# Kernel optimization log

Hardware: AMD Instinct MI355X
Metric: run time of the kernel (lower is better)

## Reference

```python
import jax, jax.numpy as jnp
import numpy as np

NUM_HEADS = 32
NUM_KV_HEADS = 8
HEAD_DIM = 128
HIDDEN = 4096
ROPE_THETA = 10000.0
SLIDING_WINDOW = 1024
NEG_INF = -1e9


def _make_sliding_window_mask(q_len, kv_len, window):
    # additive mask: 0 where attendable (causal AND within window), -inf otherwise
    i = jnp.arange(q_len)[:, None]
    j = jnp.arange(kv_len)[None, :]
    allowed = (j <= i) & (j > i - window)
    return jnp.where(allowed, 0.0, NEG_INF).astype(jnp.float32)[None, None]  # [1,1,q,kv]


def _rope_tables(seq_len, head_dim, theta):
    inv_freq = 1.0 / (theta ** (jnp.arange(0, head_dim, 2, dtype=jnp.float32) / head_dim))
    t = jnp.arange(seq_len, dtype=jnp.float32)
    freqs = jnp.einsum('i,j->ij', t, inv_freq)        # [S, D/2]
    emb = jnp.concatenate([freqs, freqs], axis=-1)     # [S, D]
    return jnp.cos(emb), jnp.sin(emb)


def _rotate_half(x):
    d = x.shape[-1] // 2
    return jnp.concatenate([-x[..., d:], x[..., :d]], axis=-1)


def setup_inputs() -> dict:
    key = jax.random.key(0)
    ks = jax.random.split(key, 5)
    B, S = 1, 2048
    sc = 0.02
    hidden_states = jax.random.normal(ks[0], (B, S, HIDDEN), dtype=jnp.float32)
    Wq = jax.random.normal(ks[1], (HIDDEN, NUM_HEADS * HEAD_DIM), dtype=jnp.float32) * sc
    Wk = jax.random.normal(ks[2], (HIDDEN, NUM_KV_HEADS * HEAD_DIM), dtype=jnp.float32) * sc
    Wv = jax.random.normal(ks[3], (HIDDEN, NUM_KV_HEADS * HEAD_DIM), dtype=jnp.float32) * sc
    Wo = jax.random.normal(ks[4], (NUM_HEADS * HEAD_DIM, HIDDEN), dtype=jnp.float32) * sc
    attention_mask = _make_sliding_window_mask(S, S, SLIDING_WINDOW)
    position_ids = jnp.arange(S, dtype=jnp.int64)[None, :]
    return {"hidden_states": hidden_states, "attention_mask": attention_mask,
            "position_ids": position_ids, "Wq": Wq, "Wk": Wk, "Wv": Wv, "Wo": Wo}


def reference(hidden_states, attention_mask, position_ids, Wq, Wk, Wv, Wo):
    B, S, _ = hidden_states.shape
    # projections
    q = (hidden_states @ Wq).reshape(B, S, NUM_HEADS, HEAD_DIM).transpose(0, 2, 1, 3)      # [B,H,S,D]
    k = (hidden_states @ Wk).reshape(B, S, NUM_KV_HEADS, HEAD_DIM).transpose(0, 2, 1, 3)   # [B,Hk,S,D]
    v = (hidden_states @ Wv).reshape(B, S, NUM_KV_HEADS, HEAD_DIM).transpose(0, 2, 1, 3)
    # RoPE
    cos_t, sin_t = _rope_tables(S, HEAD_DIM, ROPE_THETA)
    cos = cos_t[position_ids][:, None]  # [B,1,S,D]
    sin = sin_t[position_ids][:, None]
    q = q * cos + _rotate_half(q) * sin
    k = k * cos + _rotate_half(k) * sin
    # repeat_kv (GQA): [B,Hk,S,D] -> [B,H,S,D]
    n_rep = NUM_HEADS // NUM_KV_HEADS
    k = jnp.repeat(k, n_rep, axis=1)
    v = jnp.repeat(v, n_rep, axis=1)
    # attention
    scores = jnp.einsum('bhqd,bhkd->bhqk', q, k) / np.sqrt(HEAD_DIM)
    scores = scores + attention_mask
    probs = jax.nn.softmax(scores, axis=-1)
    out = jnp.einsum('bhqk,bhkd->bhqd', probs, v)
    out = out.transpose(0, 2, 1, 3).reshape(B, S, HIDDEN)
    return out @ Wo
```

## Files before the change

### kernel.cpp

```cpp
#include <hip/hip_runtime.h>

typedef __attribute__((ext_vector_type(8))) short short8;
typedef __attribute__((ext_vector_type(4))) short s16x4;
typedef __attribute__((ext_vector_type(4))) float f32x4;
typedef unsigned short u16;
typedef unsigned int u32;

__device__ __forceinline__ u16 f2bf(float f) {
  union { float f; unsigned int u; } v; v.f = f;
  unsigned int r = (v.u + 0x7FFFu + ((v.u >> 16) & 1u)) >> 16;
  return (u16)r;
}
__device__ __forceinline__ float bf2f(u16 b) {
  union { unsigned int u; float f; } v; v.u = ((unsigned int)b) << 16;
  return v.f;
}
__device__ __forceinline__ void load_lds16(const void* g, void* l) {
  __builtin_amdgcn_global_load_lds((const __attribute__((address_space(1))) void*)g,
                                   (__attribute__((address_space(3))) void*)l, 16, 0, 0);
}

__global__ void cvt_f32_bf16_kernel(const float* __restrict__ in, u16* __restrict__ out, int n4) {
  int i = blockIdx.x * blockDim.x + threadIdx.x;
  if (i >= n4) return;
  float4 v = ((const float4*)in)[i];
  ushort4 o;
  o.x = f2bf(v.x); o.y = f2bf(v.y); o.z = f2bf(v.z); o.w = f2bf(v.w);
  ((ushort4*)out)[i] = o;
}

__global__ void combine2_f32_kernel(float* __restrict__ out, const u16* __restrict__ p0,
                                    const u16* __restrict__ p1, int n8) {
  int i = blockIdx.x * blockDim.x + threadIdx.x;
  if (i >= n8) return;
  short8 a = ((const short8*)p0)[i];
  short8 b = ((const short8*)p1)[i];
  float4 o0, o1;
  o0.x = bf2f((u16)a[0]) + bf2f((u16)b[0]);
  o0.y = bf2f((u16)a[1]) + bf2f((u16)b[1]);
  o0.z = bf2f((u16)a[2]) + bf2f((u16)b[2]);
  o0.w = bf2f((u16)a[3]) + bf2f((u16)b[3]);
  o1.x = bf2f((u16)a[4]) + bf2f((u16)b[4]);
  o1.y = bf2f((u16)a[5]) + bf2f((u16)b[5]);
  o1.z = bf2f((u16)a[6]) + bf2f((u16)b[6]);
  o1.w = bf2f((u16)a[7]) + bf2f((u16)b[7]);
  ((float4*)out)[i * 2]     = o0;
  ((float4*)out)[i * 2 + 1] = o1;
}

__global__ void combine_kv_rope_kernel(const u16* __restrict__ PKV, u16* __restrict__ Kb,
                                       u16* __restrict__ Vt) {
  int i = blockIdx.x * blockDim.x + threadIdx.x;
  if (i < 131072) {
    int s = i >> 6, r = i & 63, hh = r >> 3, c = r & 7;
    size_t lo8 = (size_t)s * 128 + hh * 16 + c;
    size_t hi8 = lo8 + 8;
    float lo[8] = {0,0,0,0,0,0,0,0}, hi[8] = {0,0,0,0,0,0,0,0};
#pragma unroll
    for (int z = 0; z < 4; ++z) {
      short8 a = *(const short8*)(PKV + (size_t)z * 4194304 + lo8 * 8);
      short8 b = *(const short8*)(PKV + (size_t)z * 4194304 + hi8 * 8);
#pragma unroll
      for (int j = 0; j < 8; ++j) { lo[j] += bf2f((u16)a[j]); hi[j] += bf2f((u16)b[j]); }
    }
    short8 olo, ohi;
#pragma unroll
    for (int ii = 0; ii < 8; ++ii) {
      int j = c * 8 + ii;
      float invf = exp2f(-(float)j * (13.287712379549449f / 64.0f));
      float sn, cs;
      sincosf((float)s * invf, &sn, &cs);
      olo[ii] = (short)f2bf(lo[ii] * cs - hi[ii] * sn);
      ohi[ii] = (short)f2bf(hi[ii] * cs + lo[ii] * sn);
    }
    *(short8*)(Kb + lo8 * 8) = olo;
    *(short8*)(Kb + hi8 * 8) = ohi;
  } else {
    int v = i - 131072;
    const u16* src = PKV + 2097152;
    float sm[8] = {0,0,0,0,0,0,0,0};
#pragma unroll
    for (int z = 0; z < 4; ++z) {
      short8 a = *(const short8*)(src + (size_t)z * 4194304 + (size_t)v * 8);
#pragma unroll
      for (int j = 0; j < 8; ++j) sm[j] += bf2f((u16)a[j]);
    }
    short8 o;
#pragma unroll
    for (int j = 0; j < 8; ++j) o[j] = (short)f2bf(sm[j]);
    ((short8*)Vt)[v] = o;
  }
}

__device__ __forceinline__ void tconv64_tile(const float* __restrict__ W, u16* __restrict__ Wt,
                                             int K, int N, int nb, int kb, int tid) {
  __shared__ float tile[64][65];
  int tx = tid & 15, ty = tid >> 4;
  const float* src = W + (size_t)(kb + ty) * N + nb + tx * 4;
#pragma unroll
  for (int i = 0; i < 4; ++i) {
    float4 v = *(const float4*)(src + (size_t)i * 16 * N);
    tile[ty + i * 16][tx * 4 + 0] = v.x;
    tile[ty + i * 16][tx * 4 + 1] = v.y;
    tile[ty + i * 16][tx * 4 + 2] = v.z;
    tile[ty + i * 16][tx * 4 + 3] = v.w;
  }
  __syncthreads();
  u16* dst = Wt + (size_t)(nb + ty) * K + kb + tx * 4;
#pragma unroll
  for (int i = 0; i < 4; ++i) {
    s16x4 o;
#pragma unroll
    for (int j = 0; j < 4; ++j) o[j] = (short)f2bf(tile[tx * 4 + j][ty + i * 16]);
    *(s16x4*)(dst + (size_t)i * 16 * K) = o;
  }
}

__global__ void tconv3_kernel(const float* __restrict__ Wq, const float* __restrict__ Wk,
                              const float* __restrict__ Wv, u16* __restrict__ WqT,
                              u16* __restrict__ WkvT) {
  int id = blockIdx.x;
  if (id < 4096)      tconv64_tile(Wq, WqT, 4096, 4096, (id & 63) * 64, (id >> 6) * 64, threadIdx.x);
  else if (id < 5120) { int t = id - 4096; tconv64_tile(Wk, WkvT, 4096, 1024, (t & 15) * 64, (t >> 4) * 64, threadIdx.x); }
  else                { int t = id - 5120; tconv64_tile(Wv, WkvT + (size_t)1024 * 4096, 4096, 1024, (t & 15) * 64, (t >> 4) * 64, threadIdx.x); }
}

__global__ void tconv1_kernel(const float* __restrict__ W, u16* __restrict__ Wt) {
  int id = blockIdx.x;
  tconv64_tile(W, Wt, 4096, 4096, (id & 63) * 64, (id >> 6) * 64, threadIdx.x);
}

__global__ __launch_bounds__(512, 1) void gemm256_kernel(
    const u16* __restrict__ A, const u16* __restrict__ B,
    u16* __restrict__ C0, u16* __restrict__ C1, int N, int K, int KH) {
  __shared__ u16 As[2][256 * 64];
  __shared__ u16 Bs[2][256 * 64];
  int tid = threadIdx.x, lane = tid & 63, wid = tid >> 6;
  int wr = wid >> 2, wc = wid & 3;
  int g = lane >> 4, q = lane & 15;
  int id = blockIdx.z * gridDim.x * gridDim.y + blockIdx.y * gridDim.x + blockIdx.x;
  int tot = gridDim.x * gridDim.y * gridDim.z;
  int swz = (id & 7) * (tot >> 3) + (id >> 3);
  int perh = gridDim.x * gridDim.y;
  int z = swz / perh, rem = swz % perh;
  int m0 = (rem / gridDim.x) * 256, n0 = (rem % gridDim.x) * 256;
  int k0 = z * KH;
  f32x4 acc[8][4];
#pragma unroll
  for (int i = 0; i < 8; ++i)
#pragma unroll
    for (int j = 0; j < 4; ++j) acc[i][j] = (f32x4){0.f, 0.f, 0.f, 0.f};
  int srow = tid >> 3;
  int scol = ((tid & 7) ^ (srow & 7)) << 3;
  const u16* ga = A + (size_t)(m0 + srow) * K + k0 + scol;
  const u16* gb = B + (size_t)(n0 + srow) * K + k0 + scol;
  int xorm = (q & 7) << 3;
  int arow = wr * 128 + q;
  int brow = wc * 64 + q;
  int nt = KH >> 6;

  auto stage = [&](int buf, int t) {
    const u16* pa = ga + t * 64;
    const u16* pb = gb + t * 64;
#pragma unroll
    for (int it = 0; it < 4; ++it) {
      load_lds16(pa + (size_t)it * 64 * K, (char*)(&As[buf][0]) + it * 8192 + tid * 16);
      load_lds16(pb + (size_t)it * 64 * K, (char*)(&Bs[buf][0]) + it * 8192 + tid * 16);
    }
  };

  stage(0, 0);
  stage(1, 1);
  asm volatile("s_waitcnt vmcnt(8)" ::: "memory");
  __builtin_amdgcn_s_barrier();
  for (int t = 0; t < nt; ++t) {
    int cur = t & 1;
    int col0 = (g * 8) ^ xorm;
    short8 a0[8], b0[4];
#pragma unroll
    for (int m = 0; m < 8; ++m) a0[m] = *(const short8*)&As[cur][(arow + m * 16) * 64 + col0];
#pragma unroll
    for (int n = 0; n < 4; ++n) b0[n] = *(const short8*)&Bs[cur][(brow + n * 16) * 64 + col0];
    __builtin_amdgcn_s_setprio(1);
#pragma unroll
    for (int m = 0; m < 8; ++m)
#pragma unroll
      for (int n = 0; n < 4; ++n)
        acc[m][n] = __builtin_amdgcn_mfma_f32_16x16x32_bf16(a0[m], b0[n], acc[m][n], 0, 0, 0);
    __builtin_amdgcn_s_setprio(0);
    int col1 = (32 + g * 8) ^ xorm;
    short8 a1[8], b1[4];
#pragma unroll
    for (int m = 0; m < 8; ++m) a1[m] = *(const short8*)&As[cur][(arow + m * 16) * 64 + col1];
#pragma unroll
    for (int n = 0; n < 4; ++n) b1[n] = *(const short8*)&Bs[cur][(brow + n * 16) * 64 + col1];
    asm volatile("s_waitcnt lgkmcnt(0)" ::: "memory");
    __builtin_amdgcn_s_barrier();
    if (t + 2 < nt) stage(cur, t + 2);
    __builtin_amdgcn_sched_barrier(0);
    __builtin_amdgcn_s_setprio(1);
#pragma unroll
    for (int m = 0; m < 8; ++m)
#pragma unroll
      for (int n = 0; n < 4; ++n)
        acc[m][n] = __builtin_amdgcn_mfma_f32_16x16x32_bf16(a1[m], b1[n], acc[m][n], 0, 0, 0);
    __builtin_amdgcn_s_setprio(0);
    if (t + 2 < nt)      { asm volatile("s_waitcnt vmcnt(8)" ::: "memory"); }
    else if (t + 1 < nt) { asm volatile("s_waitcnt vmcnt(0)" ::: "memory"); }
    __builtin_amdgcn_s_barrier();
  }
  int crow = m0 + wr * 128 + g * 4;
  int ccol = n0 + wc * 64 + q;
  u16* dst = z ? C1 : C0;
#pragma unroll
  for (int fm = 0; fm < 8; ++fm)
#pragma unroll
    for (int fn = 0; fn < 4; ++fn)
#pragma unroll
      for (int r = 0; r < 4; ++r)
        dst[(size_t)(crow + fm * 16 + r) * N + ccol + fn * 16] = f2bf(acc[fm][fn][r]);
}

__global__ __launch_bounds__(512, 1) void gemm_kv256_kernel(
    const u16* __restrict__ A, const u16* __restrict__ B,
    u16* __restrict__ PKV, int K, int KH) {
  __shared__ u16 As[2][256 * 64];
  __shared__ u16 Bs[2][256 * 64];
  int tid = threadIdx.x, lane = tid & 63, wid = tid >> 6;
  int wr = wid >> 2, wc = wid & 3;
  int g = lane >> 4, q = lane & 15;
  int id = blockIdx.z * 64 + blockIdx.y * 8 + blockIdx.x;
  int swz = (id & 7) * 32 + (id >> 3);
  int z = swz >> 6, rem = swz & 63;
  int m0 = (rem >> 3) * 256, n0 = (rem & 7) * 256;
  int k0 = z * KH;
  f32x4 acc[8][4];
#pragma unroll
  for (int i = 0; i < 8; ++i)
#pragma unroll
    for (int j = 0; j < 4; ++j) acc[i][j] = (f32x4){0.f, 0.f, 0.f, 0.f};
  int srow = tid >> 3;
  int scol = ((tid & 7) ^ (srow & 7)) << 3;
  const u16* ga = A + (size_t)(m0 + srow) * K + k0 + scol;
  const u16* gb = B + (size_t)(n0 + srow) * K + k0 + scol;
  int xorm = (q & 7) << 3;
  int arow = wr * 128 + q;
  int brow = wc * 64 + q;
  int nt = KH >> 6;

  auto stage = [&](int buf, int t) {
    const u16* pa = ga + t * 64;
    const u16* pb = gb + t * 64;
#pragma unroll
    for (int it = 0; it < 4; ++it) {
      load_lds16(pa + (size_t)it * 64 * K, (char*)(&As[buf][0]) + it * 8192 + tid * 16);
      load_lds16(pb + (size_t)it * 64 * K, (char*)(&Bs[buf][0]) + it * 8192 + tid * 16);
    }
  };

  stage(0, 0);
  stage(1, 1);
  asm volatile("s_waitcnt vmcnt(8)" ::: "memory");
  __builtin_amdgcn_s_barrier();
  for (int t = 0; t < nt; ++t) {
    int cur = t & 1;
    int col0 = (g * 8) ^ xorm;
    short8 a0[8], b0[4];
#pragma unroll
    for (int m = 0; m < 8; ++m) a0[m] = *(const short8*)&As[cur][(arow + m * 16) * 64 + col0];
#pragma unroll
    for (int n = 0; n < 4; ++n) b0[n] = *(const short8*)&Bs[cur][(brow + n * 16) * 64 + col0];
    __builtin_amdgcn_s_setprio(1);
#pragma unroll
    for (int m = 0; m < 8; ++m)
#pragma unroll
      for (int n = 0; n < 4; ++n)
        acc[m][n] = __builtin_amdgcn_mfma_f32_16x16x32_bf16(a0[m], b0[n], acc[m][n], 0, 0, 0);
    __builtin_amdgcn_s_setprio(0);
    int col1 = (32 + g * 8) ^ xorm;
    short8 a1[8], b1[4];
#pragma unroll
    for (int m = 0; m < 8; ++m) a1[m] = *(const short8*)&As[cur][(arow + m * 16) * 64 + col1];
#pragma unroll
    for (int n = 0; n < 4; ++n) b1[n] = *(const short8*)&Bs[cur][(brow + n * 16) * 64 + col1];
    asm volatile("s_waitcnt lgkmcnt(0)" ::: "memory");
    __builtin_amdgcn_s_barrier();
    if (t + 2 < nt) stage(cur, t + 2);
    __builtin_amdgcn_sched_barrier(0);
    __builtin_amdgcn_s_setprio(1);
#pragma unroll
    for (int m = 0; m < 8; ++m)
#pragma unroll
      for (int n = 0; n < 4; ++n)
        acc[m][n] = __builtin_amdgcn_mfma_f32_16x16x32_bf16(a1[m], b1[n], acc[m][n], 0, 0, 0);
    __builtin_amdgcn_s_setprio(0);
    if (t + 2 < nt)      { asm volatile("s_waitcnt vmcnt(8)" ::: "memory"); }
    else if (t + 1 < nt) { asm volatile("s_waitcnt vmcnt(0)" ::: "memory"); }
    __builtin_amdgcn_s_barrier();
  }
  int crow = m0 + wr * 128 + g * 4;
  int ccol = n0 + wc * 64 + q;
  u16* Kpart = PKV + (size_t)z * 4194304;
  u16* Vpart = Kpart + 2097152;
  if (n0 < 1024) {
#pragma unroll
    for (int fm = 0; fm < 8; ++fm)
#pragma unroll
      for (int fn = 0; fn < 4; ++fn)
#pragma unroll
        for (int r = 0; r < 4; ++r)
          Kpart[(size_t)(crow + fm * 16 + r) * 1024 + ccol + fn * 16] = f2bf(acc[fm][fn][r]);
  } else {
#pragma unroll
    for (int fn = 0; fn < 4; ++fn) {
      int vcol = ccol + fn * 16 - 1024;
#pragma unroll
      for (int fm = 0; fm < 8; ++fm) {
        s16x4 o;
#pragma unroll
        for (int r = 0; r < 4; ++r) o[r] = (short)f2bf(acc[fm][fn][r]);
        *(s16x4*)(Vpart + (size_t)vcol * 2048 + crow + fm * 16) = o;
      }
    }
  }
}

__global__ __launch_bounds__(512, 4) void attn_kernel(
    const u16* __restrict__ Q0, const u16* __restrict__ Q1,
    const u16* __restrict__ Kg, const u16* __restrict__ Vt, u16* __restrict__ O) {
  __shared__ u16 Ks[2][64 * 128];
  __shared__ u16 Vs[2][128 * 64];
  int tid = threadIdx.x, lane = tid & 63, w = tid >> 6;
  int wg = w >> 2;
  int g = lane >> 4, q = lane & 15;
  int q0 = blockIdx.x * 128;
  int h = blockIdx.y, hk = h >> 2;
  int qbase = q0 + wg * 64;
  int qrow = qbase + (w & 3) * 16;
  int xorm = (lane & 7) << 3;
  short8 qf[4];
  {
    size_t qoff = (size_t)(qrow + q) * 4096 + h * 128 + g * 8;
    float sum[4][8];
#pragma unroll
    for (int kk = 0; kk < 4; ++kk) {
      short8 a = *(const short8*)(Q0 + qoff + kk * 32);
      short8 b = *(const short8*)(Q1 + qoff + kk * 32);
#pragma unroll
      for (int i = 0; i < 8; ++i) sum[kk][i] = bf2f((u16)a[i]) + bf2f((u16)b[i]);
    }
    const float scale = 0.12751781828987514f;
    float srow = (float)(qrow + q);
#pragma unroll
    for (int kk = 0; kk < 2; ++kk)
#pragma unroll
      for (int i = 0; i < 8; ++i) {
        int j = kk * 32 + g * 8 + i;
        float invf = exp2f(-(float)j * (13.287712379549449f / 64.0f));
        float sn, cs;
        sincosf(srow * invf, &sn, &cs);
        float lo = sum[kk][i], hi = sum[kk + 2][i];
        qf[kk][i]     = (short)f2bf((lo * cs - hi * sn) * scale);
        qf[kk + 2][i] = (short)f2bf((hi * cs + lo * sn) * scale);
      }
  }
  float mrow = -1e30f, lsum = 0.f;
  f32x4 of[8];
#pragma unroll
  for (int d = 0; d < 8; ++d) of[d] = (f32x4){0.f, 0.f, 0.f, 0.f};
  int bjt_lo = (q0 >= 1024) ? ((q0 - 1023) >> 6) : 0;
  int bjt_hi = (q0 + 64) >> 6;
  int wjt_lo = (qbase >= 1024) ? ((qbase - 1023) >> 6) : 0;
  int wjt_hi = qbase >> 6;
  int krow = tid >> 4;
  int kchunk = (tid & 15) ^ (krow & 7);
  const u16* kbase = Kg + (size_t)krow * 1024 + hk * 128 + (kchunk << 3);
  int vrow = tid >> 3;
  int vchunk = (tid & 7) ^ (vrow & 7);
  const u16* vbase = Vt + (size_t)(hk * 128 + vrow) * 2048 + (vchunk << 3);

  auto stageK = [&](int buf, int j0) {
    const u16* gp = kbase + (size_t)j0 * 1024;
#pragma unroll
    for (int it = 0; it < 2; ++it)
      load_lds16(gp + (size_t)it * 32 * 1024, (char*)(&Ks[buf][0]) + it * 8192 + tid * 16);
  };
  auto stageV = [&](int buf, int j0) {
    const u16* gp = vbase + j0;
#pragma unroll
    for (int it = 0; it < 2; ++it)
      load_lds16(gp + (size_t)it * 64 * 2048, (char*)(&Vs[buf][0]) + it * 8192 + tid * 16);
  };

  int cur = 0;
  stageK(0, bjt_lo << 6);
  stageV(0, bjt_lo << 6);
  asm volatile("s_waitcnt vmcnt(0)" ::: "memory");
  __syncthreads();
  for (int jt = bjt_lo; jt <= bjt_hi; ++jt) {
    int j0 = jt << 6;
    if (jt < bjt_hi) { stageK(cur ^ 1, j0 + 64); stageV(cur ^ 1, j0 + 64); }
    if (jt >= wjt_lo && jt <= wjt_hi) {
      f32x4 sf[4];
#pragma unroll
      for (int nt = 0; nt < 4; ++nt) sf[nt] = (f32x4){0.f, 0.f, 0.f, 0.f};
      const u16* ks = &Ks[cur][0];
      __builtin_amdgcn_s_setprio(1);
#pragma unroll
      for (int kk = 0; kk < 4; ++kk) {
        short8 qv = qf[kk];
        int col = (kk * 32 + g * 8) ^ xorm;
#pragma unroll
        for (int nt = 0; nt < 4; ++nt) {
          short8 kf = *(const short8*)&ks[(nt * 16 + q) * 128 + col];
          sf[nt] = __builtin_amdgcn_mfma_f32_16x16x32_bf16(kf, qv, sf[nt], 0, 0, 0);
        }
      }
      __builtin_amdgcn_s_setprio(0);
      float p[4][4];
#pragma unroll
      for (int nt = 0; nt < 4; ++nt)
#pragma unroll
        for (int r = 0; r < 4; ++r) p[nt][r] = sf[nt][r];
      if (j0 + 63 > qrow || j0 + 1009 <= qrow) {
        int qq = qrow + q;
        int kb = j0 + g * 4;
#pragma unroll
        for (int nt = 0; nt < 4; ++nt)
#pragma unroll
          for (int r = 0; r < 4; ++r) {
            int key = kb + nt * 16 + r;
            if (key > qq || key + 1024 <= qq) p[nt][r] = -1e9f;
          }
      }
      float tm = p[0][0];
#pragma unroll
      for (int nt = 0; nt < 4; ++nt)
#pragma unroll
        for (int r = 0; r < 4; ++r) tm = fmaxf(tm, p[nt][r]);
      tm = fmaxf(tm, __shfl_xor(tm, 16));
      tm = fmaxf(tm, __shfl_xor(tm, 32));
      if (__any(tm > mrow + 8.f)) {
        float nm = fmaxf(mrow, tm);
        float sc = __builtin_amdgcn_exp2f(mrow - nm);
        mrow = nm;
        lsum *= sc;
#pragma unroll
        for (int d = 0; d < 8; ++d) of[d] *= sc;
      }
      float ps = 0.f;
#pragma unroll
      for (int nt = 0; nt < 4; ++nt)
#pragma unroll
        for (int r = 0; r < 4; ++r) {
          float e = __builtin_amdgcn_exp2f(p[nt][r] - mrow);
          p[nt][r] = e;
          ps += e;
        }
      ps += __shfl_xor(ps, 16);
      ps += __shfl_xor(ps, 32);
      lsum += ps;
      u32 pk[4][2];
#pragma unroll
      for (int nt = 0; nt < 4; ++nt) {
        pk[nt][0] = __builtin_amdgcn_perm(__float_as_uint(p[nt][1]), __float_as_uint(p[nt][0]), 0x07060302u);
        pk[nt][1] = __builtin_amdgcn_perm(__float_as_uint(p[nt][3]), __float_as_uint(p[nt][2]), 0x07060302u);
      }
      int s0 = q + ((g & 1) ? 32 : 0);
      int s1 = s0 + 16;
      bool hi_sel = g >= 2;
      const u16* vs = &Vs[cur][0];
      __builtin_amdgcn_s_setprio(1);
#pragma unroll
      for (int kh = 0; kh < 2; ++kh) {
        int lo = kh * 2, hi = lo + 1;
        u32 a0 = (u32)__shfl((int)pk[lo][0], s0);
        u32 a1 = (u32)__shfl((int)pk[lo][1], s0);
        u32 b0 = (u32)__shfl((int)pk[hi][0], s0);
        u32 b1 = (u32)__shfl((int)pk[hi][1], s0);
        u32 a2 = (u32)__shfl((int)pk[lo][0], s1);
        u32 a3 = (u32)__shfl((int)pk[lo][1], s1);
        u32 b2 = (u32)__shfl((int)pk[hi][0], s1);
        u32 b3 = (u32)__shfl((int)pk[hi][1], s1);
        union { u32 u[4]; short8 s; } pb;
        pb.u[0] = hi_sel ? b0 : a0;
        pb.u[1] = hi_sel ? b1 : a1;
        pb.u[2] = hi_sel ? b2 : a2;
        pb.u[3] = hi_sel ? b3 : a3;
        int col = (kh * 32 + g * 8) ^ xorm;
#pragma unroll
        for (int dt = 0; dt < 8; ++dt) {
          short8 vv = *(const short8*)&vs[(dt * 16 + q) * 64 + col];
          of[dt] = __builtin_amdgcn_mfma_f32_16x16x32_bf16(vv, pb.s, of[dt], 0, 0, 0);
        }
      }
      __builtin_amdgcn_s_setprio(0);
    }
    asm volatile("s_waitcnt vmcnt(0)" ::: "memory");
    __builtin_amdgcn_s_barrier();
    cur ^= 1;
  }
  float inv = 1.f / lsum;
  u16* op = O + (size_t)(qrow + q) * 4096 + h * 128 + g * 4;
#pragma unroll
  for (int dt = 0; dt < 8; ++dt) {
    s16x4 o4;
#pragma unroll
    for (int r = 0; r < 4; ++r) o4[r] = (short)f2bf(of[dt][r] * inv);
    *(s16x4*)(op + dt * 16) = o4;
  }
}

extern "C" void kernel_launch(void* const* d_in, const int* in_sizes, int n_in,
                              void* d_out, int out_size, void* d_ws, size_t ws_size,
                              hipStream_t stream) {
  (void)in_sizes; (void)n_in; (void)out_size;
  const float* hs = (const float*)d_in[0];
  const float* Wq = (const float*)d_in[3];
  const float* Wk = (const float*)d_in[4];
  const float* Wv = (const float*)d_in[5];
  const float* Wo = (const float*)d_in[6];
  float* out = (float*)d_out;
  char* ws = (char*)d_ws;

  u16* Xb   = (u16*)(ws + 0);
  u16* Wt   = (u16*)(ws + 16777216);
  u16* WkvT = (u16*)(ws + 50331648);
  u16* Qb   = (u16*)(ws + 67108864);
  u16* Kb   = (u16*)(ws + 83886080);
  u16* Vtb  = (u16*)(ws + 88080384);
  u16* P1q  = (u16*)(ws + 96468992);
  u16* PKV  = Wt;
  u16* P0o  = WkvT;
  u16* P1o  = Qb;
  u16* Ao   = Xb;
  if (ws_size < 113246208u) return;

  cvt_f32_bf16_kernel<<<dim3(2097152 / 256), 256, 0, stream>>>(hs, Xb, 2097152);

  tconv3_kernel<<<dim3(6144), 256, 0, stream>>>(Wq, Wk, Wv, Wt, WkvT);

  gemm256_kernel<<<dim3(16, 8, 2), 512, 0, stream>>>(Xb, Wt, Qb, P1q, 4096, 4096, 2048);

  gemm_kv256_kernel<<<dim3(8, 8, 4), 512, 0, stream>>>(Xb, WkvT, PKV, 4096, 1024);
  combine_kv_rope_kernel<<<dim3(1536), 256, 0, stream>>>(PKV, Kb, Vtb);

  attn_kernel<<<dim3(16, 32), 512, 0, stream>>>(Qb, P1q, Kb, Vtb, Ao);

  tconv1_kernel<<<dim3(4096), 256, 0, stream>>>(Wo, Wt);
  gemm256_kernel<<<dim3(16, 8, 2), 512, 0, stream>>>(Ao, Wt, P0o, P1o, 4096, 4096, 2048);
  combine2_f32_kernel<<<dim3(4096), 256, 0, stream>>>(out, P0o, P1o, 1048576);
}
```

Before: 303.8 us.

## Precompute RoPE cos/sin table, merge prep kernels, hoist K/V staging before Q setup

Result: no change. 299.8 us (-1.3%).

```diff
diff --git a/kernel.cpp b/kernel.cpp
--- a/kernel.cpp
+++ b/kernel.cpp
@@ -20,13 +20,61 @@
                                    (__attribute__((address_space(3))) void*)l, 16, 0, 0);
 }
 
-__global__ void cvt_f32_bf16_kernel(const float* __restrict__ in, u16* __restrict__ out, int n4) {
-  int i = blockIdx.x * blockDim.x + threadIdx.x;
-  if (i >= n4) return;
-  float4 v = ((const float4*)in)[i];
-  ushort4 o;
-  o.x = f2bf(v.x); o.y = f2bf(v.y); o.z = f2bf(v.z); o.w = f2bf(v.w);
-  ((ushort4*)out)[i] = o;
+__device__ __forceinline__ void tconv64_tile(const float* __restrict__ W, u16* __restrict__ Wt,
+                                             int K, int N, int nb, int kb, int tid) {
+  __shared__ float tile[64][65];
+  int tx = tid & 15, ty = tid >> 4;
+  const float* src = W + (size_t)(kb + ty) * N + nb + tx * 4;
+#pragma unroll
+  for (int i = 0; i < 4; ++i) {
+    float4 v = *(const float4*)(src + (size_t)i * 16 * N);
+    tile[ty + i * 16][tx * 4 + 0] = v.x;
+    tile[ty + i * 16][tx * 4 + 1] = v.y;
+    tile[ty + i * 16][tx * 4 + 2] = v.z;
+    tile[ty + i * 16][tx * 4 + 3] = v.w;
+  }
+  __syncthreads();
+  u16* dst = Wt + (size_t)(nb + ty) * K + kb + tx * 4;
+#pragma unroll
+  for (int i = 0; i < 4; ++i) {
+    s16x4 o;
+#pragma unroll
+    for (int j = 0; j < 4; ++j) o[j] = (short)f2bf(tile[tx * 4 + j][ty + i * 16]);
+    *(s16x4*)(dst + (size_t)i * 16 * K) = o;
+  }
+}
+
+__global__ void prep_kernel(const float* __restrict__ Wq, const float* __restrict__ Wk,
+                            const float* __restrict__ Wv, u16* __restrict__ WqT,
+                            u16* __restrict__ WkvT, const float* __restrict__ X,
+                            u16* __restrict__ Xb, float* __restrict__ Tab) {
+  int id = blockIdx.x;
+  int tid = threadIdx.x;
+  if (id < 4096) { tconv64_tile(Wq, WqT, 4096, 4096, (id & 63) * 64, (id >> 6) * 64, tid); return; }
+  if (id < 5120) { int t = id - 4096; tconv64_tile(Wk, WkvT, 4096, 1024, (t & 15) * 64, (t >> 4) * 64, tid); return; }
+  if (id < 6144) { int t = id - 5120; tconv64_tile(Wv, WkvT + (size_t)1024 * 4096, 4096, 1024, (t & 15) * 64, (t >> 4) * 64, tid); return; }
+  if (id < 14336) {
+    int i = (id - 6144) * 256 + tid;
+    float4 v = ((const float4*)X)[i];
+    ushort4 o;
+    o.x = f2bf(v.x); o.y = f2bf(v.y); o.z = f2bf(v.z); o.w = f2bf(v.w);
+    ((ushort4*)Xb)[i] = o;
+    return;
+  }
+  {
+    int i = (id - 14336) * 256 + tid;
+    int s = i >> 6, j = i & 63;
+    float invf = exp2f(-(float)j * (13.287712379549449f / 64.0f));
+    float sn, cs;
+    sincosf((float)s * invf, &sn, &cs);
+    Tab[(size_t)s * 128 + j * 2]     = cs;
+    Tab[(size_t)s * 128 + j * 2 + 1] = sn;
+  }
+}
+
+__global__ void tconv1_kernel(const float* __restrict__ W, u16* __restrict__ Wt) {
+  int id = blockIdx.x;
+  tconv64_tile(W, Wt, 4096, 4096, (id & 63) * 64, (id >> 6) * 64, threadIdx.x);
 }
 
 __global__ void combine2_f32_kernel(float* __restrict__ out, const u16* __restrict__ p0,
@@ -49,7 +97,7 @@
 }
 
 __global__ void combine_kv_rope_kernel(const u16* __restrict__ PKV, u16* __restrict__ Kb,
-                                       u16* __restrict__ Vt) {
+                                       u16* __restrict__ Vt, const float* __restrict__ Tab) {
   int i = blockIdx.x * blockDim.x + threadIdx.x;
   if (i < 131072) {
     int s = i >> 6, r = i & 63, hh = r >> 3, c = r & 7;
@@ -63,13 +111,11 @@
 #pragma unroll
       for (int j = 0; j < 8; ++j) { lo[j] += bf2f((u16)a[j]); hi[j] += bf2f((u16)b[j]); }
     }
+    const float* tr = Tab + (size_t)s * 128 + c * 16;
     short8 olo, ohi;
 #pragma unroll
     for (int ii = 0; ii < 8; ++ii) {
-      int j = c * 8 + ii;
-      float invf = exp2f(-(float)j * (13.287712379549449f / 64.0f));
-      float sn, cs;
-      sincosf((float)s * invf, &sn, &cs);
+      float cs = tr[ii * 2], sn = tr[ii * 2 + 1];
       olo[ii] = (short)f2bf(lo[ii] * cs - hi[ii] * sn);
       ohi[ii] = (short)f2bf(hi[ii] * cs + lo[ii] * sn);
     }
@@ -90,44 +136,6 @@
     for (int j = 0; j < 8; ++j) o[j] = (short)f2bf(sm[j]);
     ((short8*)Vt)[v] = o;
   }
-}
-
-__device__ __forceinline__ void tconv64_tile(const float* __restrict__ W, u16* __restrict__ Wt,
-                                             int K, int N, int nb, int kb, int tid) {
-  __shared__ float tile[64][65];
-  int tx = tid & 15, ty = tid >> 4;
-  const float* src = W + (size_t)(kb + ty) * N + nb + tx * 4;
-#pragma unroll
-  for (int i = 0; i < 4; ++i) {
-    float4 v = *(const float4*)(src + (size_t)i * 16 * N);
-    tile[ty + i * 16][tx * 4 + 0] = v.x;
-    tile[ty + i * 16][tx * 4 + 1] = v.y;
-    tile[ty + i * 16][tx * 4 + 2] = v.z;
-    tile[ty + i * 16][tx * 4 + 3] = v.w;
-  }
-  __syncthreads();
-  u16* dst = Wt + (size_t)(nb + ty) * K + kb + tx * 4;
-#pragma unroll
-  for (int i = 0; i < 4; ++i) {
-    s16x4 o;
-#pragma unroll
-    for (int j = 0; j < 4; ++j) o[j] = (short)f2bf(tile[tx * 4 + j][ty + i * 16]);
-    *(s16x4*)(dst + (size_t)i * 16 * K) = o;
-  }
-}
-
-__global__ void tconv3_kernel(const float* __restrict__ Wq, const float* __restrict__ Wk,
-                              const float* __restrict__ Wv, u16* __restrict__ WqT,
-                              u16* __restrict__ WkvT) {
-  int id = blockIdx.x;
-  if (id < 4096)      tconv64_tile(Wq, WqT, 4096, 4096, (id & 63) * 64, (id >> 6) * 64, threadIdx.x);
-  else if (id < 5120) { int t = id - 4096; tconv64_tile(Wk, WkvT, 4096, 1024, (t & 15) * 64, (t >> 4) * 64, threadIdx.x); }
-  else                { int t = id - 5120; tconv64_tile(Wv, WkvT + (size_t)1024 * 4096, 4096, 1024, (t & 15) * 64, (t >> 4) * 64, threadIdx.x); }
-}
-
-__global__ void tconv1_kernel(const float* __restrict__ W, u16* __restrict__ Wt) {
-  int id = blockIdx.x;
-  tconv64_tile(W, Wt, 4096, 4096, (id & 63) * 64, (id >> 6) * 64, threadIdx.x);
 }
 
 __global__ __launch_bounds__(512, 1) void gemm256_kernel(
@@ -327,7 +335,8 @@
 
 __global__ __launch_bounds__(512, 4) void attn_kernel(
     const u16* __restrict__ Q0, const u16* __restrict__ Q1,
-    const u16* __restrict__ Kg, const u16* __restrict__ Vt, u16* __restrict__ O) {
+    const u16* __restrict__ Kg, const u16* __restrict__ Vt,
+    const float* __restrict__ Tab, u16* __restrict__ O) {
   __shared__ u16 Ks[2][64 * 128];
   __shared__ u16 Vs[2][128 * 64];
   int tid = threadIdx.x, lane = tid & 63, w = tid >> 6;
@@ -338,36 +347,6 @@
   int qbase = q0 + wg * 64;
   int qrow = qbase + (w & 3) * 16;
   int xorm = (lane & 7) << 3;
-  short8 qf[4];
-  {
-    size_t qoff = (size_t)(qrow + q) * 4096 + h * 128 + g * 8;
-    float sum[4][8];
-#pragma unroll
-    for (int kk = 0; kk < 4; ++kk) {
-      short8 a = *(const short8*)(Q0 + qoff + kk * 32);
-      short8 b = *(const short8*)(Q1 + qoff + kk * 32);
-#pragma unroll
-      for (int i = 0; i < 8; ++i) sum[kk][i] = bf2f((u16)a[i]) + bf2f((u16)b[i]);
-    }
-    const float scale = 0.12751781828987514f;
-    float srow = (float)(qrow + q);
-#pragma unroll
-    for (int kk = 0; kk < 2; ++kk)
-#pragma unroll
-      for (int i = 0; i < 8; ++i) {
-        int j = kk * 32 + g * 8 + i;
-        float invf = exp2f(-(float)j * (13.287712379549449f / 64.0f));
-        float sn, cs;
-        sincosf(srow * invf, &sn, &cs);
-        float lo = sum[kk][i], hi = sum[kk + 2][i];
-        qf[kk][i]     = (short)f2bf((lo * cs - hi * sn) * scale);
-        qf[kk + 2][i] = (short)f2bf((hi * cs + lo * sn) * scale);
-      }
-  }
-  float mrow = -1e30f, lsum = 0.f;
-  f32x4 of[8];
-#pragma unroll
-  for (int d = 0; d < 8; ++d) of[d] = (f32x4){0.f, 0.f, 0.f, 0.f};
   int bjt_lo = (q0 >= 1024) ? ((q0 - 1023) >> 6) : 0;
   int bjt_hi = (q0 + 64) >> 6;
   int wjt_lo = (qbase >= 1024) ? ((qbase - 1023) >> 6) : 0;
@@ -392,9 +371,38 @@
       load_lds16(gp + (size_t)it * 64 * 2048, (char*)(&Vs[buf][0]) + it * 8192 + tid * 16);
   };
 
-  int cur = 0;
   stageK(0, bjt_lo << 6);
   stageV(0, bjt_lo << 6);
+  short8 qf[4];
+  {
+    size_t qoff = (size_t)(qrow + q) * 4096 + h * 128 + g * 8;
+    float sum[4][8];
+#pragma unroll
+    for (int kk = 0; kk < 4; ++kk) {
+      short8 a = *(const short8*)(Q0 + qoff + kk * 32);
+      short8 b = *(const short8*)(Q1 + qoff + kk * 32);
+#pragma unroll
+      for (int i = 0; i < 8; ++i) sum[kk][i] = bf2f((u16)a[i]) + bf2f((u16)b[i]);
+    }
+    const float scale = 0.12751781828987514f;
+    const float* tr = Tab + (size_t)(qrow + q) * 128;
+#pragma unroll
+    for (int kk = 0; kk < 2; ++kk)
+#pragma unroll
+      for (int i = 0; i < 8; ++i) {
+        int j = kk * 32 + g * 8 + i;
+        float cs = tr[j * 2], sn = tr[j * 2 + 1];
+        float lo = sum[kk][i], hi = sum[kk + 2][i];
+        qf[kk][i]     = (short)f2bf((lo * cs - hi * sn) * scale);
+        qf[kk + 2][i] = (short)f2bf((hi * cs + lo * sn) * scale);
+      }
+  }
+  float mrow = -1e30f, lsum = 0.f;
+  f32x4 of[8];
+#pragma unroll
+  for (int d = 0; d < 8; ++d) of[d] = (f32x4){0.f, 0.f, 0.f, 0.f};
+
+  int cur = 0;
   asm volatile("s_waitcnt vmcnt(0)" ::: "memory");
   __syncthreads();
   for (int jt = bjt_lo; jt <= bjt_hi; ++jt) {
@@ -529,6 +537,7 @@
   u16* Qb   = (u16*)(ws + 67108864);
   u16* Kb   = (u16*)(ws + 83886080);
   u16* Vtb  = (u16*)(ws + 88080384);
+  float* Tab = (float*)(ws + 92274688);
   u16* P1q  = (u16*)(ws + 96468992);
   u16* PKV  = Wt;
   u16* P0o  = WkvT;
@@ -536,16 +545,14 @@
   u16* Ao   = Xb;
   if (ws_size < 113246208u) return;
 
-  cvt_f32_bf16_kernel<<<dim3(2097152 / 256), 256, 0, stream>>>(hs, Xb, 2097152);
-
-  tconv3_kernel<<<dim3(6144), 256, 0, stream>>>(Wq, Wk, Wv, Wt, WkvT);
+  prep_kernel<<<dim3(14848), 256, 0, stream>>>(Wq, Wk, Wv, Wt, WkvT, hs, Xb, Tab);
 
   gemm256_kernel<<<dim3(16, 8, 2), 512, 0, stream>>>(Xb, Wt, Qb, P1q, 4096, 4096, 2048);
 
   gemm_kv256_kernel<<<dim3(8, 8, 4), 512, 0, stream>>>(Xb, WkvT, PKV, 4096, 1024);
-  combine_kv_rope_kernel<<<dim3(1536), 256, 0, stream>>>(PKV, Kb, Vtb);
-
-  attn_kernel<<<dim3(16, 32), 512, 0, stream>>>(Qb, P1q, Kb, Vtb, Ao);
+  combine_kv_rope_kernel<<<dim3(1536), 256, 0, stream>>>(PKV, Kb, Vtb, Tab);
+
+  attn_kernel<<<dim3(16, 32), 512, 0, stream>>>(Qb, P1q, Kb, Vtb, Tab, Ao);
 
   tconv1_kernel<<<dim3(4096), 256, 0, stream>>>(Wo, Wt);
   gemm256_kernel<<<dim3(16, 8, 2), 512, 0, stream>>>(Ao, Wt, P0o, P1o, 4096, 4096, 2048);
```
